# Optimization experiments

Hardware: AMD Instinct MI355X
Metric: run time of the kernel (lower is better)

## Reference

```python
import jax, jax.numpy as jnp
import numpy as np

T, E, IN, OUT, A, R = 16384, 8, 1024, 1024, 8, 16  # tokens, experts, d_in, d_out, adapters, lora rank


def prepare_routing(x, indices, num_groups):
    """Sort tokens by group index; return sorted x, per-group counts, unsort map, sorted ids."""
    sort_idx = jnp.argsort(indices)  # stable sort keeps within-group order
    x_sorted = x[sort_idx]
    group_sizes = jnp.bincount(indices, length=num_groups).astype(jnp.int32)
    unsort_indices = jnp.argsort(sort_idx)
    return x_sorted, group_sizes, unsort_indices, indices[sort_idx]


def setup_inputs() -> dict:
    key = jax.random.key(0)
    ks = jax.random.split(key, 6)
    # tokens pre-sorted by expert: group_sizes must sum to T exactly
    expert_ids = jnp.sort(jax.random.randint(ks[0], (T,), 0, E))
    group_sizes = jnp.bincount(expert_ids, length=E).astype(jnp.int32)
    x = jax.random.normal(ks[1], (T, IN), jnp.float32)
    adapter_indices_sorted = jax.random.randint(ks[2], (T,), 0, A)
    weight = jax.random.normal(ks[3], (E, IN, OUT), jnp.float32) * 0.02
    lora_A = jax.random.normal(ks[4], (A, E, IN, R), jnp.float32) * 0.02
    lora_B = jax.random.normal(ks[5], (A, E, R, OUT), jnp.float32) * 0.02
    lora_scaling = jnp.ones((A,), jnp.float32)
    return {
        "x": x,
        "group_sizes": group_sizes,
        "adapter_indices_sorted": adapter_indices_sorted,
        "weight": weight,
        "lora_A": lora_A,
        "lora_B": lora_B,
        "lora_scaling": lora_scaling,
    }


def reference(x, group_sizes, adapter_indices_sorted, weight, lora_A, lora_B, lora_scaling):
    # base grouped GEMM over experts: [T,IN] x [E,IN,OUT] -> [T,OUT]
    base_out = jax.lax.ragged_dot(x, weight, group_sizes)

    # per-token expert id from contiguous group sizes
    expert_ids = jnp.repeat(jnp.arange(E), group_sizes, total_repeat_length=T)
    flattened = expert_ids * A + adapter_indices_sorted  # expert-major (E,A) group id

    # flatten adapters x experts into E*A groups (expert-major to match flattened ids)
    A_mat = lora_A.transpose(1, 0, 2, 3).reshape(E * A, IN, R)
    B_mat = lora_B.transpose(1, 0, 2, 3).reshape(E * A, R, OUT)

    x_sorted, combined_gs, unsort_indices, _ = prepare_routing(x, flattened, E * A)
    inter = jax.lax.ragged_dot(x_sorted, A_mat, combined_gs)          # [T,R]
    lora_out_sorted = jax.lax.ragged_dot(inter, B_mat, combined_gs)   # [T,OUT]
    lora_out = lora_out_sorted[unsort_indices]
    lora_out = lora_out * lora_scaling[adapter_indices_sorted][:, None]
    return base_out + lora_out
```

## Files before the change

### kernel.cpp

```cpp
#include <hip/hip_runtime.h>

#define T_TOK 16384
#define NEXP 8
#define DIN 1024
#define DOUT 1024
#define NADP 8
#define RANK 16
#define NGRP 64
#define MAXTILES 135
#define TILE2 64
#define MAXT2 320
#define BK 64

typedef float f32x4 __attribute__((ext_vector_type(4)));
typedef __bf16 bf16x8 __attribute__((ext_vector_type(8)));

typedef __attribute__((address_space(3))) void lds_void;
typedef __attribute__((address_space(1))) void g_void;

static __device__ __forceinline__ unsigned short f2bf(float f) {
    union { float f; unsigned u; } c; c.f = f;
    unsigned r = c.u + 0x7FFFu + ((c.u >> 16) & 1u);
    return (unsigned short)(r >> 16);
}

#define NBX 16512
#define NBW 2048
__global__ __launch_bounds__(256) void k_convert_all(const float* __restrict__ x,
                                                     const float* __restrict__ W,
                                                     const float* __restrict__ lA,
                                                     const float* __restrict__ lB,
                                                     unsigned short* __restrict__ xb,
                                                     unsigned short* __restrict__ Wt,
                                                     unsigned short* __restrict__ Agt,
                                                     unsigned short* __restrict__ Blt) {
    __shared__ __attribute__((aligned(16))) unsigned short lds_u[16 * 1032];
    int b = blockIdx.x;
    int t = threadIdx.x;
    if (b < NBX) {
        size_t i = ((size_t)b * 256 + t) * 4;
        ushort4 u;
        if (i < (size_t)T_TOK * DIN) {
            float4 v = *(const float4*)(x + i);
            u.x = f2bf(v.x); u.y = f2bf(v.y); u.z = f2bf(v.z); u.w = f2bf(v.w);
        } else {
            u.x = 0; u.y = 0; u.z = 0; u.w = 0;
        }
        *(ushort4*)(xb + i) = u;
    } else if (b < NBX + NBW) {
        int idx = b - NBX;
        int e = idx >> 8;
        int k0 = ((idx >> 4) & 15) * 64, n0 = (idx & 15) * 64;
        const float* We = W + (size_t)e * DIN * DOUT;
        unsigned short* Wte = Wt + (size_t)e * DIN * DOUT;
        int kr = t >> 2;
        int nc = (t & 3) * 16;
#pragma unroll
        for (int j = 0; j < 4; j++) {
            float4 v = *(const float4*)(We + (size_t)(k0 + kr) * DOUT + n0 + nc + j * 4);
            lds_u[(nc + j * 4 + 0) * 80 + kr] = f2bf(v.x);
            lds_u[(nc + j * 4 + 1) * 80 + kr] = f2bf(v.y);
            lds_u[(nc + j * 4 + 2) * 80 + kr] = f2bf(v.z);
            lds_u[(nc + j * 4 + 3) * 80 + kr] = f2bf(v.w);
        }
        __syncthreads();
        int n = t >> 2;
        int kk = (t & 3) * 16;
        uint4 v0 = *(const uint4*)&lds_u[n * 80 + kk];
        uint4 v1 = *(const uint4*)&lds_u[n * 80 + kk + 8];
        *(uint4*)(Wte + (size_t)(n0 + n) * DIN + k0 + kk) = v0;
        *(uint4*)(Wte + (size_t)(n0 + n) * DIN + k0 + kk + 8) = v1;
    } else if (b < NBX + NBW + NGRP) {
        int g = b - (NBX + NBW);
        int a = g & 7, e = g >> 3;
        const float* src = lA + (size_t)(a * NEXP + e) * DIN * RANK;
#pragma unroll
        for (int it = 0; it < 4; it++) {
            int k = it * 256 + t;
            const float4* p = (const float4*)(src + (size_t)k * RANK);
            float4 v0 = p[0], v1 = p[1], v2 = p[2], v3 = p[3];
            lds_u[0 * 1032 + k] = f2bf(v0.x);  lds_u[1 * 1032 + k] = f2bf(v0.y);
            lds_u[2 * 1032 + k] = f2bf(v0.z);  lds_u[3 * 1032 + k] = f2bf(v0.w);
            lds_u[4 * 1032 + k] = f2bf(v1.x);  lds_u[5 * 1032 + k] = f2bf(v1.y);
            lds_u[6 * 1032 + k] = f2bf(v1.z);  lds_u[7 * 1032 + k] = f2bf(v1.w);
            lds_u[8 * 1032 + k] = f2bf(v2.x);  lds_u[9 * 1032 + k] = f2bf(v2.y);
            lds_u[10 * 1032 + k] = f2bf(v2.z); lds_u[11 * 1032 + k] = f2bf(v2.w);
            lds_u[12 * 1032 + k] = f2bf(v3.x); lds_u[13 * 1032 + k] = f2bf(v3.y);
            lds_u[14 * 1032 + k] = f2bf(v3.z); lds_u[15 * 1032 + k] = f2bf(v3.w);
        }
        __syncthreads();
        unsigned short* dst = Agt + (size_t)g * RANK * DIN;
        int r = t >> 4, ks = (t & 15) * 64;
#pragma unroll
        for (int j = 0; j < 8; j++)
            *(uint4*)(dst + r * DIN + ks + j * 8) = *(const uint4*)&lds_u[r * 1032 + ks + j * 8];
    } else {
        int idx = b - (NBX + NBW + NGRP);
        int e = idx >> 3, nc = idx & 7;
        int k = t >> 1, half = t & 1;
        int a = k >> 4, r = k & 15;
        const float* src = lB + ((size_t)(a * NEXP + e) * RANK + r) * DOUT + nc * 128 + half * 64;
#pragma unroll
        for (int j = 0; j < 16; j++) {
            float4 v = *(const float4*)(src + j * 4);
            int nl = half * 64 + j * 4;
            lds_u[k * 129 + nl + 0] = f2bf(v.x);
            lds_u[k * 129 + nl + 1] = f2bf(v.y);
            lds_u[k * 129 + nl + 2] = f2bf(v.z);
            lds_u[k * 129 + nl + 3] = f2bf(v.w);
        }
        __syncthreads();
        int nl = t >> 1, kh = t & 1;
        unsigned short* dst = Blt + ((size_t)(e * 1024 + nc * 128 + nl)) * 128 + kh * 64;
#pragma unroll
        for (int g2 = 0; g2 < 8; g2++) {
            uint4 pv;
            unsigned short s0 = lds_u[(kh * 64 + g2 * 8 + 0) * 129 + nl];
            unsigned short s1 = lds_u[(kh * 64 + g2 * 8 + 1) * 129 + nl];
            unsigned short s2 = lds_u[(kh * 64 + g2 * 8 + 2) * 129 + nl];
            unsigned short s3 = lds_u[(kh * 64 + g2 * 8 + 3) * 129 + nl];
            unsigned short s4 = lds_u[(kh * 64 + g2 * 8 + 4) * 129 + nl];
            unsigned short s5 = lds_u[(kh * 64 + g2 * 8 + 5) * 129 + nl];
            unsigned short s6 = lds_u[(kh * 64 + g2 * 8 + 6) * 129 + nl];
            unsigned short s7 = lds_u[(kh * 64 + g2 * 8 + 7) * 129 + nl];
            pv.x = (unsigned)s0 | ((unsigned)s1 << 16);
            pv.y = (unsigned)s2 | ((unsigned)s3 << 16);
            pv.z = (unsigned)s4 | ((unsigned)s5 << 16);
            pv.w = (unsigned)s6 | ((unsigned)s7 << 16);
            *(uint4*)(dst + g2 * 8) = pv;
        }
    }
}

__global__ __launch_bounds__(1024) void k_route_all(const int* __restrict__ gs,
                                                    const int* __restrict__ aidx,
                                                    int* __restrict__ gid,
                                                    int* __restrict__ perm,
                                                    int* __restrict__ sched,
                                                    int* __restrict__ sched2) {
    __shared__ int hist[NGRP];
    __shared__ int cursor[NGRP];
    __shared__ int ebase[NEXP + 1];
    int t = threadIdx.x;
    if (t < NGRP) hist[t] = 0;
    if (t == 0) {
        int acc = 0;
        for (int i = 0; i < NEXP; i++) { ebase[i] = acc; acc += gs[i]; }
        ebase[NEXP] = acc;
    }
    __syncthreads();
    for (int i = 0; i < T_TOK / 1024; i++) {
        int tok = i * 1024 + t;
        int e = 0;
#pragma unroll
        for (int j = 1; j < NEXP; j++) e += (tok >= ebase[j]);
        int g = e * NADP + aidx[tok];
        gid[tok] = g;
        atomicAdd(&hist[g], 1);
    }
    if (t < 128) perm[T_TOK + t] = T_TOK;
    __syncthreads();
    if (t == 0) {
        int off = 0, tc = 0;
        for (int g = 0; g < NGRP; g++) {
            cursor[g] = off;
            int sz = hist[g];
            for (int m = 0; m < sz; m += TILE2) {
                sched2[tc * 4 + 0] = g;
                sched2[tc * 4 + 1] = off + m;
                sched2[tc * 4 + 2] = (sz - m) < TILE2 ? (sz - m) : TILE2;
                sched2[tc * 4 + 3] = 0;
                tc++;
            }
            off += sz;
        }
        for (; tc < MAXT2; tc++) {
            sched2[tc * 4 + 0] = 0; sched2[tc * 4 + 1] = 0;
            sched2[tc * 4 + 2] = 0; sched2[tc * 4 + 3] = 0;
        }
    } else if (t == 64) {
        int off = 0, tc = 0;
        for (int e = 0; e < NEXP; e++) {
            int sz = ebase[e + 1] - ebase[e];
            for (int m = 0; m < sz; m += 128) {
                sched[tc * 4 + 0] = e;
                sched[tc * 4 + 1] = off + m;
                sched[tc * 4 + 2] = (sz - m) < 128 ? (sz - m) : 128;
                sched[tc * 4 + 3] = 0;
                tc++;
            }
            off += sz;
        }
        for (; tc < MAXTILES; tc++) {
            sched[tc * 4 + 0] = 0; sched[tc * 4 + 1] = 0;
            sched[tc * 4 + 2] = 0; sched[tc * 4 + 3] = 0;
        }
    }
    __syncthreads();
    for (int i = 0; i < T_TOK / 1024; i++) {
        int tok = i * 1024 + t;
        int pos = atomicAdd(&cursor[gid[tok]], 1);
        perm[pos] = tok;
    }
}

__global__ __launch_bounds__(256) void k_pass1(const unsigned short* __restrict__ xb,
                                               const unsigned short* __restrict__ Agt,
                                               const int* __restrict__ sched2,
                                               const int* __restrict__ perm,
                                               float* __restrict__ inter) {
    __shared__ __attribute__((aligned(16))) unsigned short As[64 * 32];
    int g     = sched2[blockIdx.x * 4 + 0];
    int m0    = sched2[blockIdx.x * 4 + 1];
    int valid = sched2[blockIdx.x * 4 + 2];
    if (valid == 0) return;

    int t = threadIdx.x;
    int lane = t & 63, w = t >> 6;
    int ln = lane & 15, q = lane >> 4;

    const unsigned short* Ag = Agt + (size_t)g * RANK * DIN;
    int prow = perm[m0 + (t >> 2)];
    const unsigned short* ga_base = xb + (size_t)prow * DIN + (t & 3) * 8;

    f32x4 acc = (f32x4){0.f, 0.f, 0.f, 0.f};

    for (int k0 = 0; k0 < DIN; k0 += 32) {
        __syncthreads();
        __builtin_amdgcn_global_load_lds((const g_void*)(ga_base + k0),
                                         (lds_void*)((char*)As + w * 1024), 16, 0, 0);
        __syncthreads();
        bf16x8 bfr = *(const bf16x8*)(Ag + ln * DIN + k0 + q * 8);
        bf16x8 af  = *(const bf16x8*)((const char*)As + ((w * 16 + ln) * 64 + q * 16));
        acc = __builtin_amdgcn_mfma_f32_16x16x32_bf16(af, bfr, acc, 0, 0, 0);
    }
#pragma unroll
    for (int r = 0; r < 4; r++) {
        int row = w * 16 + q * 4 + r;
        if (row < valid) {
            int ptok = perm[m0 + row];
            inter[(size_t)ptok * RANK + ln] = acc[r];
        }
    }
}

__global__ __launch_bounds__(256) void k_gemm(const unsigned short* __restrict__ xb,
                                              const unsigned short* __restrict__ wt,
                                              const int* __restrict__ sched,
                                              const float* __restrict__ inter,
                                              const int* __restrict__ aidx,
                                              const float* __restrict__ scal,
                                              const unsigned short* __restrict__ Blt,
                                              float* __restrict__ out) {
    __shared__ __attribute__((aligned(16))) unsigned short smem[128 * 128];
    unsigned short* As = smem;
    unsigned short* Bs = smem + 8192;
    int e     = sched[blockIdx.y * 4 + 0];
    int m0    = sched[blockIdx.y * 4 + 1];
    int valid = sched[blockIdx.y * 4 + 2];
    if (valid == 0) return;
    int n0 = blockIdx.x * 128;

    int t = threadIdx.x;
    int lane = t & 63;
    int wave = t >> 6;
    int wm = wave >> 1, wn = wave & 1;
    int ln = lane & 15, q = lane >> 4;

    const unsigned short* wte = wt + (size_t)e * DIN * DOUT;

    f32x4 acc[4][4];
#pragma unroll
    for (int i = 0; i < 4; i++)
#pragma unroll
        for (int j = 0; j < 4; j++) acc[i][j] = (f32x4){0.f, 0.f, 0.f, 0.f};

    int srow[4], skoff[4];
#pragma unroll
    for (int j = 0; j < 4; j++) {
        srow[j]  = j * 32 + wave * 8 + (lane >> 3);
        skoff[j] = ((lane & 7) ^ (srow[j] & 7)) * 8;
    }

    for (int k0 = 0; k0 < DIN; k0 += BK) {
        __syncthreads();
#pragma unroll
        for (int j = 0; j < 4; j++) {
            __builtin_amdgcn_global_load_lds(
                (const g_void*)(xb + (size_t)(m0 + srow[j]) * DIN + k0 + skoff[j]),
                (lds_void*)((char*)As + j * 4096 + wave * 1024), 16, 0, 0);
            __builtin_amdgcn_global_load_lds(
                (const g_void*)(wte + (size_t)(n0 + srow[j]) * DIN + k0 + skoff[j]),
                (lds_void*)((char*)Bs + j * 4096 + wave * 1024), 16, 0, 0);
        }
        __syncthreads();
#pragma unroll
        for (int kf = 0; kf < 2; kf++) {
            bf16x8 af[4], bfr[4];
#pragma unroll
            for (int mi = 0; mi < 4; mi++) {
                int row = wm * 64 + mi * 16 + ln;
                int slot = (kf * 4 + q) ^ (ln & 7);
                af[mi] = *(const bf16x8*)((const char*)As + row * 128 + slot * 16);
            }
#pragma unroll
            for (int ni = 0; ni < 4; ni++) {
                int row = wn * 64 + ni * 16 + ln;
                int slot = (kf * 4 + q) ^ (ln & 7);
                bfr[ni] = *(const bf16x8*)((const char*)Bs + row * 128 + slot * 16);
            }
#pragma unroll
            for (int mi = 0; mi < 4; mi++)
#pragma unroll
                for (int ni = 0; ni < 4; ni++)
                    acc[mi][ni] = __builtin_amdgcn_mfma_f32_16x16x32_bf16(af[mi], bfr[ni], acc[mi][ni], 0, 0, 0);
        }
    }

    __syncthreads();
    {
        uint4 z = {0u, 0u, 0u, 0u};
#pragma unroll
        for (int j = 0; j < 8; j++)
            *(uint4*)((char*)smem + (j * 256 + t) * 16) = z;
    }
    __syncthreads();
    {
        int row = t >> 1, h = t & 1;
        if (row < valid) {
            int tok = m0 + row;
            int a = aidx[tok];
            float s = scal[a];
            const float* ip = inter + (size_t)tok * RANK + h * 8;
            float4 v0 = *(const float4*)ip;
            float4 v1 = *(const float4*)(ip + 4);
            unsigned short u[8];
            u[0] = f2bf(s * v0.x); u[1] = f2bf(s * v0.y); u[2] = f2bf(s * v0.z); u[3] = f2bf(s * v0.w);
            u[4] = f2bf(s * v1.x); u[5] = f2bf(s * v1.y); u[6] = f2bf(s * v1.z); u[7] = f2bf(s * v1.w);
            int slot = (a * 2 + h) ^ (row & 15);
            *(uint4*)((char*)smem + row * 256 + slot * 16) = *(uint4*)u;
        }
    }
    __syncthreads();
#pragma unroll
    for (int kf = 0; kf < 4; kf++) {
        bf16x8 af[4], bfr[4];
        const unsigned short* bbase = Blt + ((size_t)(e * 1024 + n0 + wn * 64 + ln)) * 128 + kf * 32 + q * 8;
#pragma unroll
        for (int ni = 0; ni < 4; ni++)
            bfr[ni] = *(const bf16x8*)(bbase + (size_t)ni * 16 * 128);
#pragma unroll
        for (int mi = 0; mi < 4; mi++) {
            int row = wm * 64 + mi * 16 + ln;
            int slot = (kf * 4 + q) ^ ln;
            af[mi] = *(const bf16x8*)((const char*)smem + row * 256 + slot * 16);
        }
#pragma unroll
        for (int mi = 0; mi < 4; mi++)
#pragma unroll
            for (int ni = 0; ni < 4; ni++)
                acc[mi][ni] = __builtin_amdgcn_mfma_f32_16x16x32_bf16(af[mi], bfr[ni], acc[mi][ni], 0, 0, 0);
    }

#pragma unroll
    for (int mi = 0; mi < 4; mi++) {
#pragma unroll
        for (int r = 0; r < 4; r++) {
            int row_l = wm * 64 + mi * 16 + q * 4 + r;
            if (row_l < valid) {
                float* orow = out + (size_t)(m0 + row_l) * DOUT + n0 + wn * 64 + ln;
#pragma unroll
                for (int ni = 0; ni < 4; ni++)
                    orow[ni * 16] = acc[mi][ni][r];
            }
        }
    }
}

extern "C" void kernel_launch(void* const* d_in, const int* in_sizes, int n_in,
                              void* d_out, int out_size, void* d_ws, size_t ws_size,
                              hipStream_t stream) {
    (void)in_sizes; (void)n_in; (void)out_size; (void)ws_size;
    const float* x    = (const float*)d_in[0];
    const int*   gs   = (const int*)d_in[1];
    const int*   aidx = (const int*)d_in[2];
    const float* W    = (const float*)d_in[3];
    const float* lA   = (const float*)d_in[4];
    const float* lB   = (const float*)d_in[5];
    const float* scal = (const float*)d_in[6];
    float* out = (float*)d_out;

    char* ws = (char*)d_ws;
    unsigned short* xb    = (unsigned short*)ws;            size_t o = 33816576;
    unsigned short* wt    = (unsigned short*)(ws + o);      o += 16777216;
    unsigned short* Agt   = (unsigned short*)(ws + o);      o += 2097152;
    unsigned short* Blt   = (unsigned short*)(ws + o);      o += 2097152;
    float*          inter = (float*)(ws + o);               o += 1048576;
    int*            sched = (int*)(ws + o);                 o += 2176;
    int*            sched2= (int*)(ws + o);                 o += 5120;
    int*            gid   = (int*)(ws + o);                 o += 65536;
    int*            perm  = (int*)(ws + o);                 o += 66048;

    k_convert_all<<<NBX + NBW + NGRP + 64, 256, 0, stream>>>(x, W, lA, lB, xb, wt, Agt, Blt);
    k_route_all<<<1, 1024, 0, stream>>>(gs, aidx, gid, perm, sched, sched2);
    k_pass1<<<MAXT2, 256, 0, stream>>>(xb, Agt, sched2, perm, inter);
    k_gemm<<<dim3(8, MAXTILES), 256, 0, stream>>>(xb, wt, sched, inter, aidx, scal, Blt, out);
}
```

Measured before the change: 294.4 us.

## Drop routing kernel, compute LoRA-A for all adapters per tile, double-buffer GEMM

```diff
diff --git a/kernel.cpp b/kernel.cpp
--- a/kernel.cpp
+++ b/kernel.cpp
@@ -8,8 +8,7 @@
 #define RANK 16
 #define NGRP 64
 #define MAXTILES 135
-#define TILE2 64
-#define MAXT2 320
+#define MAXP1 264
 #define BK 64
 
 typedef float f32x4 __attribute__((ext_vector_type(4)));
@@ -132,133 +131,106 @@
     }
 }
 
-__global__ __launch_bounds__(1024) void k_route_all(const int* __restrict__ gs,
-                                                    const int* __restrict__ aidx,
-                                                    int* __restrict__ gid,
-                                                    int* __restrict__ perm,
-                                                    int* __restrict__ sched,
-                                                    int* __restrict__ sched2) {
-    __shared__ int hist[NGRP];
-    __shared__ int cursor[NGRP];
-    __shared__ int ebase[NEXP + 1];
-    int t = threadIdx.x;
-    if (t < NGRP) hist[t] = 0;
-    if (t == 0) {
-        int acc = 0;
-        for (int i = 0; i < NEXP; i++) { ebase[i] = acc; acc += gs[i]; }
-        ebase[NEXP] = acc;
-    }
-    __syncthreads();
-    for (int i = 0; i < T_TOK / 1024; i++) {
-        int tok = i * 1024 + t;
-        int e = 0;
-#pragma unroll
-        for (int j = 1; j < NEXP; j++) e += (tok >= ebase[j]);
-        int g = e * NADP + aidx[tok];
-        gid[tok] = g;
-        atomicAdd(&hist[g], 1);
-    }
-    if (t < 128) perm[T_TOK + t] = T_TOK;
-    __syncthreads();
-    if (t == 0) {
-        int off = 0, tc = 0;
-        for (int g = 0; g < NGRP; g++) {
-            cursor[g] = off;
-            int sz = hist[g];
-            for (int m = 0; m < sz; m += TILE2) {
-                sched2[tc * 4 + 0] = g;
-                sched2[tc * 4 + 1] = off + m;
-                sched2[tc * 4 + 2] = (sz - m) < TILE2 ? (sz - m) : TILE2;
-                sched2[tc * 4 + 3] = 0;
-                tc++;
-            }
-            off += sz;
-        }
-        for (; tc < MAXT2; tc++) {
-            sched2[tc * 4 + 0] = 0; sched2[tc * 4 + 1] = 0;
-            sched2[tc * 4 + 2] = 0; sched2[tc * 4 + 3] = 0;
-        }
-    } else if (t == 64) {
-        int off = 0, tc = 0;
-        for (int e = 0; e < NEXP; e++) {
-            int sz = ebase[e + 1] - ebase[e];
-            for (int m = 0; m < sz; m += 128) {
-                sched[tc * 4 + 0] = e;
-                sched[tc * 4 + 1] = off + m;
-                sched[tc * 4 + 2] = (sz - m) < 128 ? (sz - m) : 128;
-                sched[tc * 4 + 3] = 0;
-                tc++;
-            }
-            off += sz;
-        }
-        for (; tc < MAXTILES; tc++) {
-            sched[tc * 4 + 0] = 0; sched[tc * 4 + 1] = 0;
-            sched[tc * 4 + 2] = 0; sched[tc * 4 + 3] = 0;
-        }
-    }
-    __syncthreads();
-    for (int i = 0; i < T_TOK / 1024; i++) {
-        int tok = i * 1024 + t;
-        int pos = atomicAdd(&cursor[gid[tok]], 1);
-        perm[pos] = tok;
-    }
-}
-
 __global__ __launch_bounds__(256) void k_pass1(const unsigned short* __restrict__ xb,
                                                const unsigned short* __restrict__ Agt,
-                                               const int* __restrict__ sched2,
-                                               const int* __restrict__ perm,
-                                               float* __restrict__ inter) {
-    __shared__ __attribute__((aligned(16))) unsigned short As[64 * 32];
-    int g     = sched2[blockIdx.x * 4 + 0];
-    int m0    = sched2[blockIdx.x * 4 + 1];
-    int valid = sched2[blockIdx.x * 4 + 2];
-    if (valid == 0) return;
+                                               const int* __restrict__ gs,
+                                               const int* __restrict__ aidx,
+                                               const float* __restrict__ scal,
+                                               unsigned short* __restrict__ interb) {
+    int bid = blockIdx.x;
+    int e = -1, m0 = 0, valid = 0;
+    {
+        int acc_t = 0, base = 0;
+#pragma unroll
+        for (int ee = 0; ee < NEXP; ee++) {
+            int sz = gs[ee];
+            int nt = (sz + 63) >> 6;
+            if (e < 0 && bid < acc_t + nt) {
+                int loc = bid - acc_t;
+                e = ee; m0 = base + (loc << 6);
+                int v = sz - (loc << 6); valid = v > 64 ? 64 : v;
+            }
+            acc_t += nt; base += sz;
+        }
+    }
+    if (e < 0) return;
 
     int t = threadIdx.x;
     int lane = t & 63, w = t >> 6;
     int ln = lane & 15, q = lane >> 4;
 
-    const unsigned short* Ag = Agt + (size_t)g * RANK * DIN;
-    int prow = perm[m0 + (t >> 2)];
-    const unsigned short* ga_base = xb + (size_t)prow * DIN + (t & 3) * 8;
-
-    f32x4 acc = (f32x4){0.f, 0.f, 0.f, 0.f};
-
+    const unsigned short* A0 = Agt + ((size_t)(e * NADP + 2 * w) * RANK + ln) * DIN + q * 8;
+    const unsigned short* A1 = A0 + (size_t)RANK * DIN;
+    const unsigned short* X0 = xb + (size_t)(m0 + ln) * DIN + q * 8;
+
+    f32x4 acc[4][2];
+#pragma unroll
+    for (int i = 0; i < 4; i++) {
+        acc[i][0] = (f32x4){0.f, 0.f, 0.f, 0.f};
+        acc[i][1] = (f32x4){0.f, 0.f, 0.f, 0.f};
+    }
+
+#pragma unroll 2
     for (int k0 = 0; k0 < DIN; k0 += 32) {
-        __syncthreads();
-        __builtin_amdgcn_global_load_lds((const g_void*)(ga_base + k0),
-                                         (lds_void*)((char*)As + w * 1024), 16, 0, 0);
-        __syncthreads();
-        bf16x8 bfr = *(const bf16x8*)(Ag + ln * DIN + k0 + q * 8);
-        bf16x8 af  = *(const bf16x8*)((const char*)As + ((w * 16 + ln) * 64 + q * 16));
-        acc = __builtin_amdgcn_mfma_f32_16x16x32_bf16(af, bfr, acc, 0, 0, 0);
-    }
-#pragma unroll
-    for (int r = 0; r < 4; r++) {
-        int row = w * 16 + q * 4 + r;
-        if (row < valid) {
-            int ptok = perm[m0 + row];
-            inter[(size_t)ptok * RANK + ln] = acc[r];
+        bf16x8 b0 = *(const bf16x8*)(A0 + k0);
+        bf16x8 b1 = *(const bf16x8*)(A1 + k0);
+#pragma unroll
+        for (int rg = 0; rg < 4; rg++) {
+            bf16x8 af = *(const bf16x8*)(X0 + (size_t)(rg * 16) * DIN + k0);
+            acc[rg][0] = __builtin_amdgcn_mfma_f32_16x16x32_bf16(b0, af, acc[rg][0], 0, 0, 0);
+            acc[rg][1] = __builtin_amdgcn_mfma_f32_16x16x32_bf16(b1, af, acc[rg][1], 0, 0, 0);
+        }
+    }
+
+    float s0 = scal[2 * w], s1 = scal[2 * w + 1];
+#pragma unroll
+    for (int rg = 0; rg < 4; rg++) {
+        int tr = rg * 16 + ln;
+        if (tr < valid) {
+            int tok = m0 + tr;
+            int a = aidx[tok];
+            if (a == 2 * w) {
+                f32x4 v = acc[rg][0];
+                ushort4 u;
+                u.x = f2bf(s0 * v[0]); u.y = f2bf(s0 * v[1]);
+                u.z = f2bf(s0 * v[2]); u.w = f2bf(s0 * v[3]);
+                *(ushort4*)(interb + (size_t)tok * RANK + q * 4) = u;
+            } else if (a == 2 * w + 1) {
+                f32x4 v = acc[rg][1];
+                ushort4 u;
+                u.x = f2bf(s1 * v[0]); u.y = f2bf(s1 * v[1]);
+                u.z = f2bf(s1 * v[2]); u.w = f2bf(s1 * v[3]);
+                *(ushort4*)(interb + (size_t)tok * RANK + q * 4) = u;
+            }
         }
     }
 }
 
 __global__ __launch_bounds__(256) void k_gemm(const unsigned short* __restrict__ xb,
                                               const unsigned short* __restrict__ wt,
-                                              const int* __restrict__ sched,
-                                              const float* __restrict__ inter,
+                                              const int* __restrict__ gs,
+                                              const unsigned short* __restrict__ interb,
                                               const int* __restrict__ aidx,
-                                              const float* __restrict__ scal,
                                               const unsigned short* __restrict__ Blt,
                                               float* __restrict__ out) {
-    __shared__ __attribute__((aligned(16))) unsigned short smem[128 * 128];
-    unsigned short* As = smem;
-    unsigned short* Bs = smem + 8192;
-    int e     = sched[blockIdx.y * 4 + 0];
-    int m0    = sched[blockIdx.y * 4 + 1];
-    int valid = sched[blockIdx.y * 4 + 2];
-    if (valid == 0) return;
+    __shared__ __attribute__((aligned(16))) unsigned short smem[32768];
+    int tileid = blockIdx.y;
+    int e = -1, m0 = 0, valid = 0;
+    {
+        int acc_t = 0, base = 0;
+#pragma unroll
+        for (int ee = 0; ee < NEXP; ee++) {
+            int sz = gs[ee];
+            int nt = (sz + 127) >> 7;
+            if (e < 0 && tileid < acc_t + nt) {
+                int loc = tileid - acc_t;
+                e = ee; m0 = base + (loc << 7);
+                int v = sz - (loc << 7); valid = v > 128 ? 128 : v;
+            }
+            acc_t += nt; base += sz;
+        }
+    }
+    if (e < 0) return;
     int n0 = blockIdx.x * 128;
 
     int t = threadIdx.x;
@@ -282,18 +254,21 @@
         skoff[j] = ((lane & 7) ^ (srow[j] & 7)) * 8;
     }
 
-    for (int k0 = 0; k0 < DIN; k0 += BK) {
-        __syncthreads();
+    auto STAGE = [&](int buf, int k0) {
 #pragma unroll
         for (int j = 0; j < 4; j++) {
             __builtin_amdgcn_global_load_lds(
                 (const g_void*)(xb + (size_t)(m0 + srow[j]) * DIN + k0 + skoff[j]),
-                (lds_void*)((char*)As + j * 4096 + wave * 1024), 16, 0, 0);
+                (lds_void*)((char*)smem + buf * 32768 + j * 4096 + wave * 1024), 16, 0, 0);
             __builtin_amdgcn_global_load_lds(
                 (const g_void*)(wte + (size_t)(n0 + srow[j]) * DIN + k0 + skoff[j]),
-                (lds_void*)((char*)Bs + j * 4096 + wave * 1024), 16, 0, 0);
-        }
-        __syncthreads();
+                (lds_void*)((char*)smem + buf * 32768 + 16384 + j * 4096 + wave * 1024), 16, 0, 0);
+        }
+    };
+
+    auto COMPUTE = [&](int buf) {
+        const char* Ab = (const char*)smem + buf * 32768;
+        const char* Bb = Ab + 16384;
 #pragma unroll
         for (int kf = 0; kf < 2; kf++) {
             bf16x8 af[4], bfr[4];
@@ -301,13 +276,13 @@
             for (int mi = 0; mi < 4; mi++) {
                 int row = wm * 64 + mi * 16 + ln;
                 int slot = (kf * 4 + q) ^ (ln & 7);
-                af[mi] = *(const bf16x8*)((const char*)As + row * 128 + slot * 16);
+                af[mi] = *(const bf16x8*)(Ab + row * 128 + slot * 16);
             }
 #pragma unroll
             for (int ni = 0; ni < 4; ni++) {
                 int row = wn * 64 + ni * 16 + ln;
                 int slot = (kf * 4 + q) ^ (ln & 7);
-                bfr[ni] = *(const bf16x8*)((const char*)Bs + row * 128 + slot * 16);
+                bfr[ni] = *(const bf16x8*)(Bb + row * 128 + slot * 16);
             }
 #pragma unroll
             for (int mi = 0; mi < 4; mi++)
@@ -315,30 +290,37 @@
                 for (int ni = 0; ni < 4; ni++)
                     acc[mi][ni] = __builtin_amdgcn_mfma_f32_16x16x32_bf16(af[mi], bfr[ni], acc[mi][ni], 0, 0, 0);
         }
-    }
-
+    };
+
+    STAGE(0, 0);
     __syncthreads();
-    {
-        uint4 z = {0u, 0u, 0u, 0u};
-#pragma unroll
-        for (int j = 0; j < 8; j++)
-            *(uint4*)((char*)smem + (j * 256 + t) * 16) = z;
-    }
+    int cur = 0;
+    for (int k0 = BK; k0 < DIN; k0 += BK) {
+        STAGE(cur ^ 1, k0);
+        COMPUTE(cur);
+        __syncthreads();
+        cur ^= 1;
+    }
+    COMPUTE(cur);
+
     __syncthreads();
     {
         int row = t >> 1, h = t & 1;
+        int rs = row & 15;
+        uint4 z = {0u, 0u, 0u, 0u};
+        uint4 payload = z;
+        int pslot = -1;
         if (row < valid) {
             int tok = m0 + row;
             int a = aidx[tok];
-            float s = scal[a];
-            const float* ip = inter + (size_t)tok * RANK + h * 8;
-            float4 v0 = *(const float4*)ip;
-            float4 v1 = *(const float4*)(ip + 4);
-            unsigned short u[8];
-            u[0] = f2bf(s * v0.x); u[1] = f2bf(s * v0.y); u[2] = f2bf(s * v0.z); u[3] = f2bf(s * v0.w);
-            u[4] = f2bf(s * v1.x); u[5] = f2bf(s * v1.y); u[6] = f2bf(s * v1.z); u[7] = f2bf(s * v1.w);
-            int slot = (a * 2 + h) ^ (row & 15);
-            *(uint4*)((char*)smem + row * 256 + slot * 16) = *(uint4*)u;
+            payload = *(const uint4*)(interb + (size_t)tok * RANK + h * 8);
+            pslot = a * 2 + h;
+        }
+#pragma unroll
+        for (int l2 = 0; l2 < 8; l2++) {
+            int l = l2 * 2 + h;
+            int phys = l ^ rs;
+            *(uint4*)((char*)smem + row * 256 + phys * 16) = (l == pslot) ? payload : z;
         }
     }
     __syncthreads();
@@ -391,18 +373,13 @@
     float* out = (float*)d_out;
 
     char* ws = (char*)d_ws;
-    unsigned short* xb    = (unsigned short*)ws;            size_t o = 33816576;
-    unsigned short* wt    = (unsigned short*)(ws + o);      o += 16777216;
-    unsigned short* Agt   = (unsigned short*)(ws + o);      o += 2097152;
-    unsigned short* Blt   = (unsigned short*)(ws + o);      o += 2097152;
-    float*          inter = (float*)(ws + o);               o += 1048576;
-    int*            sched = (int*)(ws + o);                 o += 2176;
-    int*            sched2= (int*)(ws + o);                 o += 5120;
-    int*            gid   = (int*)(ws + o);                 o += 65536;
-    int*            perm  = (int*)(ws + o);                 o += 66048;
+    unsigned short* xb     = (unsigned short*)ws;        size_t o = 33816576;
+    unsigned short* wt     = (unsigned short*)(ws + o);  o += 16777216;
+    unsigned short* Agt    = (unsigned short*)(ws + o);  o += 2097152;
+    unsigned short* Blt    = (unsigned short*)(ws + o);  o += 2097152;
+    unsigned short* interb = (unsigned short*)(ws + o);  o += 524288;
 
     k_convert_all<<<NBX + NBW + NGRP + 64, 256, 0, stream>>>(x, W, lA, lB, xb, wt, Agt, Blt);
-    k_route_all<<<1, 1024, 0, stream>>>(gs, aidx, gid, perm, sched, sched2);
-    k_pass1<<<MAXT2, 256, 0, stream>>>(xb, Agt, sched2, perm, inter);
-    k_gemm<<<dim3(8, MAXTILES), 256, 0, stream>>>(xb, wt, sched, inter, aidx, scal, Blt, out);
-}
+    k_pass1<<<MAXP1, 256, 0, stream>>>(xb, Agt, gs, aidx, scal, interb);
+    k_gemm<<<dim3(8, MAXTILES), 256, 0, stream>>>(xb, wt, gs, interb, aidx, Blt, out);
+}
```

Measured after the change: 278.6 us. 1.06x faster.
